# Kernel optimization log

Measured on AMD Instinct MI355X. Metric: run time of the kernel, lower is better.

Reference implementation:

```python
import jax, jax.numpy as jnp
import numpy as np

LN_EPS = 1e-5


def _layernorm(h, g, b):
    mu = jnp.mean(h, axis=-1, keepdims=True)
    var = jnp.var(h, axis=-1, keepdims=True)
    return (h - mu) / jnp.sqrt(var + LN_EPS) * g + b


def setup_inputs() -> dict:
    key = jax.random.key(0)
    ks = jax.random.split(key, 16)
    B, N, C, T = 32, 1024, 64, 24
    K, Fc, Ft = 3, 64, 64

    def xav(k, shape):
        lim = (6.0 / (shape[-2] + shape[-1])) ** 0.5
        return jax.random.uniform(k, shape, jnp.float32, -lim, lim)

    return {
        "x": jax.random.normal(ks[0], (B, N, C, T), jnp.float32),
        "cheb": jax.random.normal(ks[1], (K, N, N), jnp.float32) / np.float32(N) ** 0.5,
        "U1": jax.random.uniform(ks[2], (N,), jnp.float32),
        "U2": xav(ks[3], (C, N)),
        "U3": jax.random.uniform(ks[4], (C,), jnp.float32),
        "b_e": xav(ks[5], (1, T, T)),
        "V_e": xav(ks[6], (T, T)),
        "W1": jax.random.uniform(ks[7], (T,), jnp.float32),
        "W2": xav(ks[8], (C, T)),
        "W3": jax.random.uniform(ks[9], (C,), jnp.float32),
        "b_s": xav(ks[10], (1, N, N)),
        "V_s": xav(ks[11], (N, N)),
        "Theta": xav(ks[12], (K, C, Fc)),
        "tc_w": jax.random.normal(ks[13], (Ft, Fc, 1, 3), jnp.float32) * 0.05,
        "tc_b": jnp.zeros((Ft,), jnp.float32),
        "rc_w": jax.random.normal(ks[14], (Ft, C, 1, 1), jnp.float32) * 0.05,
        "rc_b": jnp.zeros((Ft,), jnp.float32),
        "ln_g": jnp.ones((Ft,), jnp.float32),
        "ln_b": jnp.zeros((Ft,), jnp.float32),
    }


def reference(x, cheb, U1, U2, U3, b_e, V_e, W1, W2, W3, b_s, V_s,
              Theta, tc_w, tc_b, rc_w, rc_b, ln_g, ln_b):
    B, N, C, T = x.shape
    K = Theta.shape[0]

    # ---- temporal attention: E (B,T,T), softmax over axis 1 ----
    lhs_t = jnp.einsum('bnct,n->btc', x, U1) @ U2            # (B,T,N)
    rhs_t = jnp.einsum('c,bnct->bnt', U3, x)                 # (B,N,T)
    prod_t = jnp.einsum('btn,bnu->btu', lhs_t, rhs_t)        # (B,T,T)
    E = jnp.einsum('bik,jk->bij', jax.nn.sigmoid(prod_t + b_e), V_e)
    E = jax.nn.softmax(E, axis=1)

    # ---- apply temporal attention ----
    x_TAt = jnp.einsum('bft,btu->bfu', x.reshape(B, N * C, T), E)
    x_TAt = x_TAt.reshape(B, N, C, T)

    # ---- spatial attention: S (B,N,N), softmax over axis 1 ----
    lhs_s = jnp.einsum('bnct,t->bnc', x_TAt, W1) @ W2        # (B,N,T)
    rhs_s = jnp.einsum('c,bnct->btn', W3, x_TAt)             # (B,T,N)
    prod_s = jnp.einsum('bnt,btm->bnm', lhs_s, rhs_s)        # (B,N,N)
    S = jnp.einsum('bik,jk->bij', jax.nn.sigmoid(prod_s + b_s), V_s)
    S = jax.nn.softmax(S, axis=1)

    # ---- K-order Chebyshev conv with spatial attention ----
    out = jnp.zeros((B, N, Theta.shape[2], T), x.dtype)
    for k in range(K):
        Tk_at = cheb[k] * S                                   # (B,N,N)
        # rhs[b,i,c,t] = sum_m Tk_at[b,m,i] * x[b,m,c,t]
        rhs = jnp.einsum('bmi,bmct->bict', Tk_at, x)
        out = out + jnp.einsum('bict,cf->bift', rhs, Theta[k])
    spatial_gcn = jax.nn.relu(out)                            # (B,N,Fc,T)

    # ---- time conv (1x3, pad (0,1)) on (B,Fc,N,T) ----
    tci = jnp.transpose(spatial_gcn, (0, 2, 1, 3))            # (B,Fc,N,T)
    tco = jax.lax.conv_general_dilated(
        tci, tc_w, window_strides=(1, 1), padding=((0, 0), (1, 1)),
        dimension_numbers=('NCHW', 'OIHW', 'NCHW'))
    tco = tco + tc_b[None, :, None, None]
    tco = jnp.transpose(tco, (0, 2, 1, 3))                    # (B,N,Ft,T)

    # ---- residual 1x1 conv on raw x ----
    rci = jnp.transpose(x, (0, 2, 1, 3))                      # (B,C,N,T)
    rco = jax.lax.conv_general_dilated(
        rci, rc_w, window_strides=(1, 1), padding=((0, 0), (0, 0)),
        dimension_numbers=('NCHW', 'OIHW', 'NCHW'))
    rco = rco + rc_b[None, :, None, None]
    rco = jnp.transpose(rco, (0, 2, 1, 3))                    # (B,N,Ft,T)

    out = jax.nn.relu(rco + tco)                              # (B,N,Ft,T)
    out = _layernorm(jnp.transpose(out, (0, 1, 3, 2)), ln_g, ln_b)
    return jnp.transpose(out, (0, 1, 3, 2))                   # (B,N,Ft,T)
```

## Files before the change

### kernel.cpp

```cpp
#include <hip/hip_runtime.h>

typedef __attribute__((ext_vector_type(8))) short short8;
typedef __attribute__((ext_vector_type(4))) float f32x4;

constexpr int B_ = 32;
constexpr int N_ = 1024;
constexpr int C_ = 64;
constexpr int T_ = 24;
constexpr int F_ = 64;
constexpr int CT_ = C_ * T_;
constexpr int KS_ = 3072;

__device__ __forceinline__ float sigmoidf_(float x) {
    return 1.0f / (1.0f + __expf(-x));
}
__device__ __forceinline__ unsigned short f2b(float f) {
    union { float f; unsigned u; } v; v.f = f;
    unsigned r = v.u + 0x7FFFu + ((v.u >> 16) & 1u);
    return (unsigned short)(r >> 16);
}
__device__ __forceinline__ float b2f(unsigned short h) {
    union { unsigned u; float f; } v; v.u = ((unsigned)h) << 16; return v.f;
}
__device__ __forceinline__ void gload_lds16(const unsigned short* g, unsigned short* l) {
    __builtin_amdgcn_global_load_lds(
        (const __attribute__((address_space(1))) unsigned int*)g,
        (__attribute__((address_space(3))) unsigned int*)l, 16, 0, 0);
}

__global__ __launch_bounds__(256) void k_rhs_t(const float* __restrict__ x,
        const float* __restrict__ U3, float* __restrict__ rhs_t) {
    int b = blockIdx.y, n0 = blockIdx.x * 8;
    int tid = threadIdx.x;
    __shared__ float xr[8 * CT_];
    __shared__ float u3s[C_];
    if (tid < C_) u3s[tid] = U3[tid];
    const float4* x4 = (const float4*)(x + ((size_t)(b * N_ + n0)) * CT_);
#pragma unroll
    for (int e = 0; e < 12; ++e) {
        int i4 = e * 256 + tid;
        float4 v = x4[i4];
        int i = i4 * 4;
        xr[i] = v.x; xr[i + 1] = v.y; xr[i + 2] = v.z; xr[i + 3] = v.w;
    }
    __syncthreads();
    if (tid < 192) {
        int n = tid / 24, t = tid % 24;
        const float* xn = xr + n * CT_ + t;
        float acc = 0.f;
#pragma unroll
        for (int c = 0; c < C_; ++c) acc += u3s[c] * xn[c * 24];
        rhs_t[((size_t)(b * N_ + n0 + n)) * T_ + t] = acc;
    }
}

__global__ void k_lhs_partial(const float* __restrict__ x, const float* __restrict__ U1,
                              float* __restrict__ partial) {
    int b = blockIdx.y, chunk = blockIdx.x;
    int tid = threadIdx.x;
    float acc[6] = {0, 0, 0, 0, 0, 0};
    int n0 = chunk * 64;
    for (int nn = 0; nn < 64; ++nn) {
        int n = n0 + nn;
        float u = U1[n];
        const float* xp = x + ((size_t)(b * N_ + n)) * CT_;
#pragma unroll
        for (int e = 0; e < 6; ++e) acc[e] += u * xp[tid + e * 256];
    }
    float* pp = partial + ((size_t)(b * 16 + chunk)) * CT_;
#pragma unroll
    for (int e = 0; e < 6; ++e) pp[tid + e * 256] = acc[e];
}

__global__ void k_lhs_reduce(const float* __restrict__ partial, float* __restrict__ lhs_t0) {
    int idx = blockIdx.x * 256 + threadIdx.x;
    if (idx >= B_ * CT_) return;
    int b = idx / CT_, flat = idx % CT_;
    float acc = 0.f;
#pragma unroll
    for (int ch = 0; ch < 16; ++ch) acc += partial[((size_t)(b * 16 + ch)) * CT_ + flat];
    lhs_t0[idx] = acc;
}

__global__ void k_lhs_t(const float* __restrict__ lhs_t0, const float* __restrict__ U2,
                        float* __restrict__ lhs_t) {
    int idx = blockIdx.x * 256 + threadIdx.x;
    if (idx >= B_ * T_ * N_) return;
    int n2 = idx % N_;
    int t = (idx / N_) % T_;
    int b = idx / (T_ * N_);
    const float* l0 = lhs_t0 + (size_t)b * CT_;
    float acc = 0.f;
#pragma unroll
    for (int c = 0; c < C_; ++c) acc += l0[c * T_ + t] * U2[c * N_ + n2];
    lhs_t[idx] = acc;
}

__global__ void k_temporal_E(const float* __restrict__ lhs_t, const float* __restrict__ rhs_t,
                             const float* __restrict__ b_e, const float* __restrict__ V_e,
                             float* __restrict__ E) {
    int b = blockIdx.x;
    int tid = threadIdx.x;
    int i = tid / T_, u = tid % T_;
    __shared__ float sig[T_][T_];
    __shared__ float e0s[T_][T_];
    __shared__ float mcol[T_], scol[T_];
    const float* lt = lhs_t + (size_t)b * T_ * N_ + (size_t)i * N_;
    const float* rt = rhs_t + (size_t)b * N_ * T_ + u;
    float acc = 0.f;
    for (int n = 0; n < N_; ++n) acc += lt[n] * rt[(size_t)n * T_];
    sig[i][u] = sigmoidf_(acc + b_e[i * T_ + u]);
    __syncthreads();
    int j = u;
    float e0 = 0.f;
#pragma unroll
    for (int kk = 0; kk < T_; ++kk) e0 += sig[i][kk] * V_e[j * T_ + kk];
    e0s[i][j] = e0;
    __syncthreads();
    if (tid < T_) {
        float mx = -1e30f;
        for (int ii = 0; ii < T_; ++ii) mx = fmaxf(mx, e0s[ii][tid]);
        float s = 0.f;
        for (int ii = 0; ii < T_; ++ii) s += __expf(e0s[ii][tid] - mx);
        mcol[tid] = mx; scol[tid] = s;
    }
    __syncthreads();
    E[(size_t)b * T_ * T_ + i * T_ + j] = __expf(e0s[i][j] - mcol[j]) / scol[j];
}

__global__ __launch_bounds__(256) void k_tspatial(const float* __restrict__ x,
        const float* __restrict__ E, const float* __restrict__ W1g,
        const float* __restrict__ W2, const float* __restrict__ W3g,
        float* __restrict__ lhs_s, float* __restrict__ rhs_s,
        unsigned short* __restrict__ xTt) {
    int b = blockIdx.y;
    int n0 = blockIdx.x * 4;
    int tid = threadIdx.x;
    __shared__ float Es[T_ * T_];
    __shared__ float W1s[T_];
    __shared__ float W2s[C_ * T_];
    __shared__ float xr[4][64][25];
    __shared__ float l0s[4][64];
    for (int e = tid; e < T_ * T_; e += 256) Es[e] = E[(size_t)b * T_ * T_ + e];
    for (int e = tid; e < C_ * T_; e += 256) W2s[e] = W2[e];
    if (tid < T_) W1s[tid] = W1g[tid];
    size_t base = ((size_t)b * N_ + n0) * CT_;
    const float4* x4 = (const float4*)(x + base);
#pragma unroll
    for (int i = 0; i < 6; ++i) {
        int e4 = i * 256 + tid;
        float4 v = x4[e4];
        int e = e4 * 4;
        int nl = e / CT_; int rem = e - nl * CT_; int c = rem / 24; int tl = rem - c * 24;
        xr[nl][c][tl] = v.x; xr[nl][c][tl + 1] = v.y;
        xr[nl][c][tl + 2] = v.z; xr[nl][c][tl + 3] = v.w;
    }
    __syncthreads();
    int nl = tid >> 6, c = tid & 63;
    float xv[T_];
#pragma unroll
    for (int t = 0; t < T_; ++t) xv[t] = xr[nl][c][t];
#pragma unroll
    for (int i = 0; i < 24; ++i) {
        int idx = i * 256 + tid;
        int cc = idx & 63, nn = (idx >> 6) & 3, t = idx >> 8;
        xTt[((size_t)(b * T_ + t) * N_ + n0 + nn) * 64 + cc] = f2b(xr[nn][cc][t]);
    }
    float w3 = W3g[c];
    float u[T_];
#pragma unroll
    for (int j = 0; j < T_; ++j) {
        float a = 0.f;
#pragma unroll
        for (int t = 0; t < T_; ++t) a += xv[t] * Es[t * T_ + j];
        u[j] = a;
    }
    float l0 = 0.f;
#pragma unroll
    for (int j = 0; j < T_; ++j) l0 += u[j] * W1s[j];
    __syncthreads();
#pragma unroll
    for (int j = 0; j < T_; ++j) xr[nl][c][j] = w3 * u[j];
    l0s[nl][c] = l0;
    __syncthreads();
    if (tid < 4 * T_) {
        int t = tid % T_, g = tid / T_;
        float racc = 0.f, lacc = 0.f;
        for (int cc = 0; cc < 64; ++cc) {
            racc += xr[g][cc][t];
            lacc += l0s[g][cc] * W2s[cc * T_ + t];
        }
        rhs_s[((size_t)b * T_ + t) * N_ + n0 + g] = racc;
        lhs_s[((size_t)(b * N_ + n0 + g)) * T_ + t] = lacc;
    }
}

__global__ void k_cvt_vs(const float* __restrict__ v, unsigned short* __restrict__ o) {
    int i = blockIdx.x * 256 + threadIdx.x;
    o[i] = f2b(v[i]);
}

__global__ void k_wcat(const float* __restrict__ tc_w, const float* __restrict__ rc_w,
                       unsigned short* __restrict__ Wcat) {
    int i = blockIdx.x * 256 + threadIdx.x;
    if (i >= F_ * 256) return;
    int ft = i >> 8, k = i & 255;
    int sel = k >> 6, c = k & 63;
    float v = (sel < 3) ? tc_w[(ft * C_ + c) * 3 + sel] : rc_w[ft * C_ + c];
    Wcat[i] = f2b(v);
}

__global__ void k_thp(const float* __restrict__ Theta, unsigned short* __restrict__ Thp) {
    int i = blockIdx.x * 256 + threadIdx.x;
    if (i >= 192 * 64) return;
    int kf = i >> 6, c = i & 63;
    int k = kf >> 6, f = kf & 63;
    Thp[i] = f2b(Theta[((size_t)k * 64 + c) * 64 + f]);
}

__global__ __launch_bounds__(256) void k_sig(const float* __restrict__ lhs_s,
        const float* __restrict__ rhs_s, const float* __restrict__ b_s,
        unsigned short* __restrict__ sigA) {
    int b = blockIdx.z, i0 = blockIdx.y * 64, k0 = blockIdx.x * 256;
    int tid = threadIdx.x;
    __shared__ float lh[64 * T_];
    __shared__ float rh[T_][256];
    for (int e = tid; e < 64 * T_; e += 256) lh[e] = lhs_s[((size_t)b * N_ + i0) * T_ + e];
#pragma unroll
    for (int t = 0; t < T_; ++t) rh[t][tid] = rhs_s[((size_t)b * T_ + t) * N_ + k0 + tid];
    __syncthreads();
    int kg = k0 + tid;
    for (int ii = 0; ii < 64; ++ii) {
        float acc = b_s[(size_t)(i0 + ii) * N_ + kg];
#pragma unroll
        for (int t = 0; t < T_; ++t) acc += lh[ii * T_ + t] * rh[t][tid];
        sigA[((size_t)b * N_ + i0 + ii) * N_ + kg] = f2b(sigmoidf_(acc));
    }
}

__global__ __launch_bounds__(256) void k_yTmm(const unsigned short* __restrict__ xTt,
        const unsigned short* __restrict__ Thp, unsigned short* __restrict__ yT) {
    int bt = blockIdx.y;
    int b = bt / T_, t = bt - b * T_;
    int m0 = blockIdx.x * 128;
    int tid = threadIdx.x;
    int lane = tid & 63, wv = tid >> 6;
    __shared__ __align__(16) char smem[50688];
    unsigned short* Asb = (unsigned short*)smem;
    unsigned short* Bsb = (unsigned short*)(smem + 24576);
    unsigned short* Cl  = (unsigned short*)(smem + 24576);
#pragma unroll
    for (int e = 0; e < 6; ++e) {
        int chunk = e * 256 + tid;
        int row = chunk >> 3, slot = chunk & 7;
        int gslot = slot ^ (row & 7);
        gload_lds16(Thp + row * 64 + gslot * 8, &Asb[chunk * 8]);
    }
    const unsigned short* Bg = xTt + ((size_t)bt * N_ + m0) * 64;
#pragma unroll
    for (int e = 0; e < 4; ++e) {
        int chunk = e * 256 + tid;
        int row = chunk >> 3, slot = chunk & 7;
        int gslot = slot ^ (row & 7);
        gload_lds16(Bg + (size_t)row * 64 + gslot * 8, &Bsb[chunk * 8]);
    }
    __syncthreads();

    short8 bf[2][2];
#pragma unroll
    for (int ni = 0; ni < 2; ++ni)
#pragma unroll
        for (int kk = 0; kk < 2; ++kk) {
            int r = wv * 32 + ni * 16 + (lane & 15);
            int slot = (kk * 4 + (lane >> 4)) ^ (r & 7);
            bf[ni][kk] = *(const short8*)&Bsb[r * 64 + slot * 8];
        }
    f32x4 acc[12][2];
#pragma unroll
    for (int mi = 0; mi < 12; ++mi)
#pragma unroll
        for (int ni = 0; ni < 2; ++ni) acc[mi][ni] = (f32x4){0.f, 0.f, 0.f, 0.f};
#pragma unroll
    for (int mi = 0; mi < 12; ++mi) {
        short8 af[2];
#pragma unroll
        for (int kk = 0; kk < 2; ++kk) {
            int r = mi * 16 + (lane & 15);
            int slot = (kk * 4 + (lane >> 4)) ^ (r & 7);
            af[kk] = *(const short8*)&Asb[r * 64 + slot * 8];
        }
#pragma unroll
        for (int kk = 0; kk < 2; ++kk)
#pragma unroll
            for (int ni = 0; ni < 2; ++ni)
                acc[mi][ni] = __builtin_amdgcn_mfma_f32_16x16x32_bf16(
                    af[kk], bf[ni][kk], acc[mi][ni], 0, 0, 0);
    }
#pragma unroll
    for (int h = 0; h < 2; ++h) {
        __syncthreads();
#pragma unroll
        for (int mi2 = 0; mi2 < 6; ++mi2) {
            int mi = h * 6 + mi2;
#pragma unroll
            for (int r = 0; r < 4; ++r) {
                int row = mi2 * 16 + (lane >> 4) * 4 + r;
#pragma unroll
                for (int ni = 0; ni < 2; ++ni)
                    Cl[row * 136 + wv * 32 + ni * 16 + (lane & 15)] = f2b(acc[mi][ni][r]);
            }
        }
        __syncthreads();
#pragma unroll
        for (int e = 0; e < 6; ++e) {
            int idx = e * 256 + tid;
            int row = idx >> 4, seg = idx & 15;
            int kf = h * 96 + row;
            int k = kf >> 6, f = kf & 63;
            uint4 v = *(const uint4*)&Cl[row * 136 + seg * 8];
            *(uint4*)&yT[((size_t)b * CT_ + f * T_ + t) * KS_ + k * N_ + m0 + seg * 8] = v;
        }
    }
}

__global__ void k_smstats(const float* __restrict__ S, float2* __restrict__ mst) {
    int b = blockIdx.y;
    int jj = threadIdx.x % 64;
    int ig = threadIdx.x / 64;
    int j = blockIdx.x * 64 + jj;
    __shared__ float rm[4][64], rs[4][64];
    float m = -1e30f, s = 0.f;
    for (int i = ig; i < N_; i += 4) {
        float v = S[((size_t)b * N_ + i) * N_ + j];
        float mn = fmaxf(m, v);
        s = s * __expf(m - mn) + __expf(v - mn);
        m = mn;
    }
    rm[ig][jj] = m; rs[ig][jj] = s;
    __syncthreads();
    if (ig == 0) {
        float M = rm[0][jj], SS = rs[0][jj];
#pragma unroll
        for (int g = 1; g < 4; ++g) {
            float mg = rm[g][jj];
            float mn = fmaxf(M, mg);
            SS = SS * __expf(M - mn) + rs[g][jj] * __expf(mg - mn);
            M = mn;
        }
        mst[(size_t)b * N_ + j] = make_float2(M, 1.f / SS);
    }
}

__global__ __launch_bounds__(256) void k_chebSt(const float* __restrict__ cheb,
        const float* __restrict__ S, const float2* __restrict__ mst,
        unsigned short* __restrict__ cs) {
    int b = blockIdx.z, i0 = blockIdx.y * 64, m0 = blockIdx.x * 64;
    int tid = threadIdx.x;
    __shared__ float st[64][65];
    __shared__ float cb[64][65];
    __shared__ float2 sst[64];
    if (tid < 64) sst[tid] = mst[(size_t)b * N_ + i0 + tid];
#pragma unroll
    for (int e = 0; e < 4; ++e) {
        int idx4 = e * 256 + tid;
        int mm = idx4 >> 4, ii0 = (idx4 & 15) * 4;
        float4 v = *(const float4*)&S[((size_t)b * N_ + m0 + mm) * N_ + i0 + ii0];
        st[mm][ii0] = v.x; st[mm][ii0 + 1] = v.y; st[mm][ii0 + 2] = v.z; st[mm][ii0 + 3] = v.w;
    }
    for (int k = 0; k < 3; ++k) {
        __syncthreads();
#pragma unroll
        for (int e = 0; e < 4; ++e) {
            int idx4 = e * 256 + tid;
            int mm = idx4 >> 4, ii0 = (idx4 & 15) * 4;
            float4 v = *(const float4*)&cheb[((size_t)k * N_ + m0 + mm) * N_ + i0 + ii0];
            cb[mm][ii0] = v.x; cb[mm][ii0 + 1] = v.y; cb[mm][ii0 + 2] = v.z; cb[mm][ii0 + 3] = v.w;
        }
        __syncthreads();
#pragma unroll
        for (int e = 0; e < 16; ++e) {
            int idx = e * 256 + tid; int mm = idx & 63, ii = idx >> 6;
            float sm = __expf(st[mm][ii] - sst[ii].x) * sst[ii].y;
            cs[((size_t)b * N_ + i0 + ii) * KS_ + k * N_ + m0 + mm] =
                f2b(sm * cb[mm][ii]);
        }
    }
}

__global__ __launch_bounds__(512, 2) void k_gemm256(
        const unsigned short* __restrict__ A, long lda, long sA,
        const unsigned short* __restrict__ Bt, long ldb, long sB,
        float* __restrict__ Cc, long ldc, long sC, int K, int nbx, int nby) {
    __shared__ __align__(16) unsigned short As[2][256 * 64];
    __shared__ __align__(16) unsigned short Bs[2][256 * 64];
    int tid = threadIdx.x;
    int lane = tid & 63, w = tid >> 6;
    int wy = w >> 2, wx = w & 3;

    int nwg = gridDim.x;
    int cpx = nwg >> 3;
    int logical = (blockIdx.x & 7) * cpx + (blockIdx.x >> 3);
    int tpb = nbx * nby;
    int b = logical / tpb;
    int tile = logical % tpb;
    int i0 = (tile / nbx) * 256;
    int j0 = (tile % nbx) * 256;

    const unsigned short* Ab = A + (size_t)b * sA + (size_t)i0 * lda;
    const unsigned short* Bb = Bt + (size_t)b * sB + (size_t)j0 * ldb;

    auto STAGE = [&](int kt, int d) {
        int kof = kt << 6;
#pragma unroll
        for (int e = 0; e < 4; ++e) {
            int chunk = e * 512 + tid;
            int row = chunk >> 3, slot = chunk & 7;
            int gslot = slot ^ (row & 7);
            gload_lds16(Ab + (size_t)row * lda + kof + gslot * 8, &As[d][chunk * 8]);
        }
#pragma unroll
        for (int e = 0; e < 4; ++e) {
            int chunk = e * 512 + tid;
            int row = chunk >> 3, slot = chunk & 7;
            int gslot = slot ^ (row & 7);
            gload_lds16(Bb + (size_t)row * ldb + kof + gslot * 8, &Bs[d][chunk * 8]);
        }
    };
    auto READF = [&](short8* af, short8* bfv,
                     const unsigned short* Asb, const unsigned short* Bsb, int kkb) {
#pragma unroll
        for (int mi = 0; mi < 8; ++mi) {
            int r = wy * 128 + mi * 16 + (lane & 15);
            int slot = (kkb + (lane >> 4)) ^ (r & 7);
            af[mi] = *(const short8*)&Asb[r * 64 + slot * 8];
        }
#pragma unroll
        for (int ni = 0; ni < 4; ++ni) {
            int r = wx * 64 + ni * 16 + (lane & 15);
            int slot = (kkb + (lane >> 4)) ^ (r & 7);
            bfv[ni] = *(const short8*)&Bsb[r * 64 + slot * 8];
        }
    };

    f32x4 acc[8][4];
#pragma unroll
    for (int mi = 0; mi < 8; ++mi)
#pragma unroll
        for (int ni = 0; ni < 4; ++ni) acc[mi][ni] = (f32x4){0.f, 0.f, 0.f, 0.f};

    int nt = K >> 6;
    STAGE(0, 0);
    STAGE(1, 1);
    asm volatile("s_waitcnt vmcnt(8)" ::: "memory");
    __builtin_amdgcn_s_barrier();
    __builtin_amdgcn_sched_barrier(0);

    short8 a0[8], b0[4], a1[8], b1[4];
    READF(a0, b0, As[0], Bs[0], 0);

    for (int kt = 0; kt < nt; ++kt) {
        int cur = kt & 1;
        READF(a1, b1, As[cur], Bs[cur], 4);
        __builtin_amdgcn_s_setprio(1);
#pragma unroll
        for (int mi = 0; mi < 8; ++mi)
#pragma unroll
            for (int ni = 0; ni < 4; ++ni)
                acc[mi][ni] = __builtin_amdgcn_mfma_f32_16x16x32_bf16(
                    a0[mi], b0[ni], acc[mi][ni], 0, 0, 0);
        __builtin_amdgcn_s_setprio(0);
        asm volatile("s_waitcnt lgkmcnt(0)" ::: "memory");
        __builtin_amdgcn_sched_barrier(0);
        __builtin_amdgcn_s_barrier();
        __builtin_amdgcn_sched_barrier(0);
        if (kt + 2 < nt) STAGE(kt + 2, cur);
        __builtin_amdgcn_sched_barrier(0);
        __builtin_amdgcn_s_setprio(1);
#pragma unroll
        for (int mi = 0; mi < 8; ++mi)
#pragma unroll
            for (int ni = 0; ni < 4; ++ni)
                acc[mi][ni] = __builtin_amdgcn_mfma_f32_16x16x32_bf16(
                    a1[mi], b1[ni], acc[mi][ni], 0, 0, 0);
        __builtin_amdgcn_s_setprio(0);
        if (kt + 2 < nt) {
            asm volatile("s_waitcnt vmcnt(8)" ::: "memory");
        } else {
            asm volatile("s_waitcnt vmcnt(0)" ::: "memory");
        }
        __builtin_amdgcn_s_barrier();
        __builtin_amdgcn_sched_barrier(0);
        if (kt + 1 < nt)
            READF(a0, b0, As[cur ^ 1], Bs[cur ^ 1], 0);
    }

    float* Cb = Cc + (size_t)b * sC;
#pragma unroll
    for (int mi = 0; mi < 8; ++mi) {
#pragma unroll
        for (int r = 0; r < 4; ++r) {
            int i = i0 + wy * 128 + mi * 16 + (lane >> 4) * 4 + r;
            float* cp = Cb + (size_t)i * ldc + j0 + wx * 64 + (lane & 15);
#pragma unroll
            for (int ni = 0; ni < 4; ++ni) cp[ni * 16] = acc[mi][ni][r];
        }
    }
}

__global__ __launch_bounds__(256) void k_final(const float* __restrict__ x,
        const float* __restrict__ sgin, const unsigned short* __restrict__ Wcat,
        const float* __restrict__ tc_b, const float* __restrict__ rc_b,
        const float* __restrict__ ln_g, const float* __restrict__ ln_b,
        float* __restrict__ out) {
    int b = blockIdx.y;
    int n0 = blockIdx.x * 4;
    int tid = threadIdx.x;
    int lane = tid & 63, wv = tid >> 6;

    __shared__ __align__(16) char smem[25600];
    unsigned short* sgb = (unsigned short*)smem;
    unsigned short* xb  = (unsigned short*)(smem + 13312);
    float* Cl = (float*)smem;
    __shared__ float tbs[64], gs[64], bbs[64];
    __shared__ float mus[96], rss[96];

    if (tid < 64) {
        tbs[tid] = tc_b[tid] + rc_b[tid];
        gs[tid] = ln_g[tid];
        bbs[tid] = ln_b[tid];
    }
    for (int e = tid; e < 512; e += 256) {
        int nl = e >> 7, r = (e >> 6) & 1, c = e & 63;
        int tt = r ? 25 : 0;
        sgb[(nl * 26 + tt) * 64 + (((c >> 3) ^ (tt & 7)) << 3) + (c & 7)] = 0;
    }
    size_t base = ((size_t)b * N_ + n0) * CT_;
    const float4* sg4 = (const float4*)(sgin + base);
    const float4* xg4 = (const float4*)(x + base);
#pragma unroll
    for (int i = 0; i < 6; ++i) {
        int e4 = i * 256 + tid;
        float4 sv4 = sg4[e4];
        float4 xv4 = xg4[e4];
        int e = e4 * 4;
        int nl = e / CT_;
        int rem = e - nl * CT_;
        int c = rem / 24;
        int tl = rem - c * 24;
        float sv[4] = {sv4.x, sv4.y, sv4.z, sv4.w};
        float xv[4] = {xv4.x, xv4.y, xv4.z, xv4.w};
#pragma unroll
        for (int j = 0; j < 4; ++j) {
            int tt = tl + j + 1;
            sgb[(nl * 26 + tt) * 64 + (((c >> 3) ^ (tt & 7)) << 3) + (c & 7)] =
                f2b(fmaxf(sv[j], 0.f));
            int tj = tl + j;
            xb[(nl * 24 + tj) * 64 + (((c >> 3) ^ (tj & 7)) << 3) + (c & 7)] = f2b(xv[j]);
        }
    }

    int ft = wv * 16 + (lane & 15);
    int g4 = lane >> 4;
    short8 bfr[8];
#pragma unroll
    for (int ks = 0; ks < 8; ++ks)
        bfr[ks] = *(const short8*)&Wcat[ft * 256 + ks * 32 + g4 * 8];

    int rnl[6], rt[6];
#pragma unroll
    for (int mi = 0; mi < 6; ++mi) {
        int row = mi * 16 + (lane & 15);
        rnl[mi] = row / 24;
        rt[mi] = row - rnl[mi] * 24;
    }

    __syncthreads();

    f32x4 acc[6];
#pragma unroll
    for (int mi = 0; mi < 6; ++mi) acc[mi] = (f32x4){0.f, 0.f, 0.f, 0.f};
#pragma unroll
    for (int mi = 0; mi < 6; ++mi) {
        int nl = rnl[mi], t = rt[mi];
#pragma unroll
        for (int ks = 0; ks < 8; ++ks) {
            const int sel = ks >> 1;
            int slot = (ks & 1) * 4 + g4;
            short8 af;
            if (sel < 3) {
                int tt = t + sel;
                af = *(const short8*)&sgb[(nl * 26 + tt) * 64 + ((slot ^ (tt & 7)) << 3)];
            } else {
                af = *(const short8*)&xb[(nl * 24 + t) * 64 + ((slot ^ (t & 7)) << 3)];
            }
            acc[mi] = __builtin_amdgcn_mfma_f32_16x16x32_bf16(af, bfr[ks], acc[mi], 0, 0, 0);
        }
    }

    __syncthreads();
#pragma unroll
    for (int mi = 0; mi < 6; ++mi)
#pragma unroll
        for (int r = 0; r < 4; ++r)
            Cl[(mi * 16 + (lane >> 4) * 4 + r) * 66 + wv * 16 + (lane & 15)] = acc[mi][r];
    __syncthreads();

    if (tid < 96) {
        float s = 0.f, s2 = 0.f;
#pragma unroll
        for (int f = 0; f < 64; ++f) {
            float v = fmaxf(Cl[tid * 66 + f] + tbs[f], 0.f);
            s += v; s2 += v * v;
        }
        float mu = s * (1.f / 64.f);
        float var = s2 * (1.f / 64.f) - mu * mu;
        mus[tid] = mu;
        rss[tid] = rsqrtf(var + 1e-5f);
    }
    __syncthreads();

    float4* o4 = (float4*)(out + base);
#pragma unroll
    for (int i = 0; i < 6; ++i) {
        int e4 = i * 256 + tid;
        int e = e4 * 4;
        int nl = e / CT_;
        int rem = e - nl * CT_;
        int f = rem / 24;
        int t0v = rem - f * 24;
        float g = gs[f], bb2 = bbs[f], tb2 = tbs[f];
        float vals[4];
#pragma unroll
        for (int j = 0; j < 4; ++j) {
            int row = nl * 24 + t0v + j;
            float v = fmaxf(Cl[row * 66 + f] + tb2, 0.f);
            vals[j] = (v - mus[row]) * rss[row] * g + bb2;
        }
        float4 r;
        r.x = vals[0]; r.y = vals[1]; r.z = vals[2]; r.w = vals[3];
        o4[e4] = r;
    }
}

extern "C" void kernel_launch(void* const* d_in, const int* in_sizes, int n_in,
                              void* d_out, int out_size, void* d_ws, size_t ws_size,
                              hipStream_t stream) {
    const float* x    = (const float*)d_in[0];
    const float* cheb = (const float*)d_in[1];
    const float* U1   = (const float*)d_in[2];
    const float* U2   = (const float*)d_in[3];
    const float* U3   = (const float*)d_in[4];
    const float* b_e  = (const float*)d_in[5];
    const float* V_e  = (const float*)d_in[6];
    const float* W1   = (const float*)d_in[7];
    const float* W2   = (const float*)d_in[8];
    const float* W3   = (const float*)d_in[9];
    const float* b_s  = (const float*)d_in[10];
    const float* V_s  = (const float*)d_in[11];
    const float* Theta= (const float*)d_in[12];
    const float* tc_w = (const float*)d_in[13];
    const float* tc_b = (const float*)d_in[14];
    const float* rc_w = (const float*)d_in[15];
    const float* rc_b = (const float*)d_in[16];
    const float* ln_g = (const float*)d_in[17];
    const float* ln_b = (const float*)d_in[18];
    float* out = (float*)d_out;

    char* base = (char*)d_ws;
    size_t o = 0;
    auto alloc = [&](size_t bytes) { size_t r = o; o += (bytes + 255) & ~(size_t)255; return r; };
    float* lhs_t   = (float*)(base + alloc((size_t)B_ * T_ * N_ * 4));
    float* rhs_t   = (float*)(base + alloc((size_t)B_ * N_ * T_ * 4));
    float* Ebuf    = (float*)(base + alloc((size_t)B_ * T_ * T_ * 4));
    float* partial = (float*)(base + alloc((size_t)B_ * 16 * CT_ * 4));
    float* lhs_t0  = (float*)(base + alloc((size_t)B_ * CT_ * 4));
    float* lhs_s   = (float*)(base + alloc((size_t)B_ * N_ * T_ * 4));
    float* rhs_s   = (float*)(base + alloc((size_t)B_ * T_ * N_ * 4));
    unsigned short* V_sb = (unsigned short*)(base + alloc((size_t)N_ * N_ * 2));
    unsigned short* Wcat = (unsigned short*)(base + alloc((size_t)F_ * 256 * 2));
    unsigned short* Thp  = (unsigned short*)(base + alloc((size_t)192 * 64 * 2));
    float2* mstats = (float2*)(base + alloc((size_t)B_ * N_ * 8));
    size_t regA = alloc((size_t)B_ * N_ * KS_ * 2);
    size_t regB = alloc((size_t)B_ * CT_ * KS_ * 2);
    unsigned short* xTt    = (unsigned short*)(base + regA);
    unsigned short* chebSt = (unsigned short*)(base + regA);
    unsigned short* sigA   = (unsigned short*)(base + regB);
    unsigned short* yT     = (unsigned short*)(base + regB);
    float* Sb  = out;
    float* gcn = out;

    dim3 b256(256);
    k_cvt_vs<<<dim3(N_ * N_ / 256), b256, 0, stream>>>(V_s, V_sb);
    k_wcat<<<dim3((F_ * 256 + 255) / 256), b256, 0, stream>>>(tc_w, rc_w, Wcat);
    k_thp<<<dim3((192 * 64 + 255) / 256), b256, 0, stream>>>(Theta, Thp);
    k_rhs_t<<<dim3(N_ / 8, B_), b256, 0, stream>>>(x, U3, rhs_t);
    k_lhs_partial<<<dim3(16, B_), b256, 0, stream>>>(x, U1, partial);
    k_lhs_reduce<<<dim3((B_ * CT_) / 256), b256, 0, stream>>>(partial, lhs_t0);
    k_lhs_t<<<dim3((B_ * T_ * N_) / 256), b256, 0, stream>>>(lhs_t0, U2, lhs_t);
    k_temporal_E<<<dim3(B_), dim3(576), 0, stream>>>(lhs_t, rhs_t, b_e, V_e, Ebuf);
    k_tspatial<<<dim3(N_ / 4, B_), b256, 0, stream>>>(x, Ebuf, W1, W2, W3,
                                                      lhs_s, rhs_s, xTt);
    k_sig<<<dim3(N_ / 256, N_ / 64, B_), b256, 0, stream>>>(lhs_s, rhs_s, b_s, sigA);
    k_gemm256<<<dim3(B_ * 4 * 4), dim3(512), 0, stream>>>(
        sigA, N_, (long)N_ * N_, V_sb, N_, 0, Sb, N_, (long)N_ * N_, N_, 4, 4);
    k_smstats<<<dim3(N_ / 64, B_), b256, 0, stream>>>(Sb, mstats);
    k_yTmm<<<dim3(N_ / 128, B_ * T_), b256, 0, stream>>>(xTt, Thp, yT);
    k_chebSt<<<dim3(N_ / 64, N_ / 64, B_), b256, 0, stream>>>(cheb, Sb, mstats, chebSt);
    k_gemm256<<<dim3(B_ * 4 * 6), dim3(512), 0, stream>>>(
        chebSt, KS_, (long)N_ * KS_, yT, KS_, (long)CT_ * KS_,
        gcn, CT_, (long)N_ * CT_, KS_, 6, 4);
    k_final<<<dim3(N_ / 4, B_), b256, 0, stream>>>(x, gcn, Wcat, tc_b, rc_b,
                                                   ln_g, ln_b, out);
}
```

Baseline: 1.154 ms.

## Fuse x reductions into one pass and parallelize temporal product over chunks

Merges the U3 and U1 reductions over x into a single kernel that stages x tiles in shared memory, so the large x tensor is read once instead of twice. The prod_t contraction over N is moved out of the 32-block temporal kernel into a chunked kernel with 8 chunks per batch, and the small partials are summed before the sigmoid and softmax. This adds a kernel launch and a larger partial buffer, and gives the fused kernel fewer blocks.

New measurement: 1.067 ms. 7.6% less time.

```diff
diff --git a/kernel.cpp b/kernel.cpp
--- a/kernel.cpp
+++ b/kernel.cpp
@@ -28,48 +28,46 @@
         (__attribute__((address_space(3))) unsigned int*)l, 16, 0, 0);
 }
 
-__global__ __launch_bounds__(256) void k_rhs_t(const float* __restrict__ x,
-        const float* __restrict__ U3, float* __restrict__ rhs_t) {
-    int b = blockIdx.y, n0 = blockIdx.x * 8;
+__global__ __launch_bounds__(256) void k_xreduce(const float* __restrict__ x,
+        const float* __restrict__ U1, const float* __restrict__ U3,
+        float* __restrict__ rhs_t, float* __restrict__ partial) {
+    int b = blockIdx.y, g0 = blockIdx.x * 32;
     int tid = threadIdx.x;
     __shared__ float xr[8 * CT_];
     __shared__ float u3s[C_];
     if (tid < C_) u3s[tid] = U3[tid];
-    const float4* x4 = (const float4*)(x + ((size_t)(b * N_ + n0)) * CT_);
-#pragma unroll
-    for (int e = 0; e < 12; ++e) {
-        int i4 = e * 256 + tid;
-        float4 v = x4[i4];
-        int i = i4 * 4;
-        xr[i] = v.x; xr[i + 1] = v.y; xr[i + 2] = v.z; xr[i + 3] = v.w;
-    }
-    __syncthreads();
-    if (tid < 192) {
-        int n = tid / 24, t = tid % 24;
-        const float* xn = xr + n * CT_ + t;
-        float acc = 0.f;
-#pragma unroll
-        for (int c = 0; c < C_; ++c) acc += u3s[c] * xn[c * 24];
-        rhs_t[((size_t)(b * N_ + n0 + n)) * T_ + t] = acc;
-    }
-}
-
-__global__ void k_lhs_partial(const float* __restrict__ x, const float* __restrict__ U1,
-                              float* __restrict__ partial) {
-    int b = blockIdx.y, chunk = blockIdx.x;
-    int tid = threadIdx.x;
-    float acc[6] = {0, 0, 0, 0, 0, 0};
-    int n0 = chunk * 64;
-    for (int nn = 0; nn < 64; ++nn) {
-        int n = n0 + nn;
-        float u = U1[n];
-        const float* xp = x + ((size_t)(b * N_ + n)) * CT_;
-#pragma unroll
-        for (int e = 0; e < 6; ++e) acc[e] += u * xp[tid + e * 256];
-    }
-    float* pp = partial + ((size_t)(b * 16 + chunk)) * CT_;
-#pragma unroll
-    for (int e = 0; e < 6; ++e) pp[tid + e * 256] = acc[e];
+    float pacc[6] = {0, 0, 0, 0, 0, 0};
+    for (int ph = 0; ph < 4; ++ph) {
+        int n0 = g0 + ph * 8;
+        __syncthreads();
+        const float4* x4 = (const float4*)(x + ((size_t)(b * N_ + n0)) * CT_);
+#pragma unroll
+        for (int e = 0; e < 12; ++e) {
+            int i4 = e * 256 + tid;
+            float4 v = x4[i4];
+            int i = i4 * 4;
+            xr[i] = v.x; xr[i + 1] = v.y; xr[i + 2] = v.z; xr[i + 3] = v.w;
+        }
+        __syncthreads();
+        if (tid < 192) {
+            int n = tid / 24, t = tid % 24;
+            const float* xn = xr + n * CT_ + t;
+            float acc = 0.f;
+#pragma unroll
+            for (int c = 0; c < C_; ++c) acc += u3s[c] * xn[c * 24];
+            rhs_t[((size_t)(b * N_ + n0 + n)) * T_ + t] = acc;
+        }
+#pragma unroll
+        for (int n = 0; n < 8; ++n) {
+            float u = U1[n0 + n];
+            const float* xn = xr + n * CT_;
+#pragma unroll
+            for (int e = 0; e < 6; ++e) pacc[e] += u * xn[tid + e * 256];
+        }
+    }
+    float* pp = partial + ((size_t)(b * 32 + blockIdx.x)) * CT_;
+#pragma unroll
+    for (int e = 0; e < 6; ++e) pp[tid + e * 256] = pacc[e];
 }
 
 __global__ void k_lhs_reduce(const float* __restrict__ partial, float* __restrict__ lhs_t0) {
@@ -78,7 +76,7 @@
     int b = idx / CT_, flat = idx % CT_;
     float acc = 0.f;
 #pragma unroll
-    for (int ch = 0; ch < 16; ++ch) acc += partial[((size_t)(b * 16 + ch)) * CT_ + flat];
+    for (int ch = 0; ch < 32; ++ch) acc += partial[((size_t)(b * 32 + ch)) * CT_ + flat];
     lhs_t0[idx] = acc;
 }
 
@@ -96,7 +94,31 @@
     lhs_t[idx] = acc;
 }
 
-__global__ void k_temporal_E(const float* __restrict__ lhs_t, const float* __restrict__ rhs_t,
+__global__ __launch_bounds__(576) void k_prodt(const float* __restrict__ lhs_t,
+        const float* __restrict__ rhs_t, float* __restrict__ ptp) {
+    int b = blockIdx.y, ch = blockIdx.x;
+    int tid = threadIdx.x;
+    __shared__ float lt[24][128];
+    __shared__ float rt[128][25];
+    int n0 = ch * 128;
+    for (int e = tid; e < 24 * 128; e += 576) {
+        int i = e >> 7, nn = e & 127;
+        lt[i][nn] = lhs_t[((size_t)b * T_ + i) * N_ + n0 + nn];
+    }
+    const float* rg = rhs_t + ((size_t)b * N_ + n0) * T_;
+    for (int e = tid; e < 128 * 24; e += 576) {
+        int nn = e / 24, t = e - nn * 24;
+        rt[nn][t] = rg[e];
+    }
+    __syncthreads();
+    int i = tid / 24, u = tid - (tid / 24) * 24;
+    float acc = 0.f;
+#pragma unroll 8
+    for (int nn = 0; nn < 128; ++nn) acc += lt[i][nn] * rt[nn][u];
+    ptp[(((size_t)b * 8 + ch) * 24 + i) * 24 + u] = acc;
+}
+
+__global__ void k_temporal_E(const float* __restrict__ ptp,
                              const float* __restrict__ b_e, const float* __restrict__ V_e,
                              float* __restrict__ E) {
     int b = blockIdx.x;
@@ -105,10 +127,10 @@
     __shared__ float sig[T_][T_];
     __shared__ float e0s[T_][T_];
     __shared__ float mcol[T_], scol[T_];
-    const float* lt = lhs_t + (size_t)b * T_ * N_ + (size_t)i * N_;
-    const float* rt = rhs_t + (size_t)b * N_ * T_ + u;
     float acc = 0.f;
-    for (int n = 0; n < N_; ++n) acc += lt[n] * rt[(size_t)n * T_];
+#pragma unroll
+    for (int ch = 0; ch < 8; ++ch)
+        acc += ptp[(((size_t)b * 8 + ch) * 24 + i) * 24 + u];
     sig[i][u] = sigmoidf_(acc + b_e[i * T_ + u]);
     __syncthreads();
     int j = u;
@@ -672,7 +694,8 @@
     float* lhs_t   = (float*)(base + alloc((size_t)B_ * T_ * N_ * 4));
     float* rhs_t   = (float*)(base + alloc((size_t)B_ * N_ * T_ * 4));
     float* Ebuf    = (float*)(base + alloc((size_t)B_ * T_ * T_ * 4));
-    float* partial = (float*)(base + alloc((size_t)B_ * 16 * CT_ * 4));
+    float* partial = (float*)(base + alloc((size_t)B_ * 32 * CT_ * 4));
+    float* ptp     = (float*)(base + alloc((size_t)B_ * 8 * T_ * T_ * 4));
     float* lhs_t0  = (float*)(base + alloc((size_t)B_ * CT_ * 4));
     float* lhs_s   = (float*)(base + alloc((size_t)B_ * N_ * T_ * 4));
     float* rhs_s   = (float*)(base + alloc((size_t)B_ * T_ * N_ * 4));
@@ -693,11 +716,11 @@
     k_cvt_vs<<<dim3(N_ * N_ / 256), b256, 0, stream>>>(V_s, V_sb);
     k_wcat<<<dim3((F_ * 256 + 255) / 256), b256, 0, stream>>>(tc_w, rc_w, Wcat);
     k_thp<<<dim3((192 * 64 + 255) / 256), b256, 0, stream>>>(Theta, Thp);
-    k_rhs_t<<<dim3(N_ / 8, B_), b256, 0, stream>>>(x, U3, rhs_t);
-    k_lhs_partial<<<dim3(16, B_), b256, 0, stream>>>(x, U1, partial);
-    k_lhs_reduce<<<dim3((B_ * CT_) / 256), b256, 0, stream>>>(partial, lhs_t0);
+    k_xreduce<<<dim3(N_ / 32, B_), b256, 0, stream>>>(x, U1, U3, rhs_t, partial);
+    k_lhs_reduce<<<dim3((B_ * CT_ + 255) / 256), b256, 0, stream>>>(partial, lhs_t0);
     k_lhs_t<<<dim3((B_ * T_ * N_) / 256), b256, 0, stream>>>(lhs_t0, U2, lhs_t);
-    k_temporal_E<<<dim3(B_), dim3(576), 0, stream>>>(lhs_t, rhs_t, b_e, V_e, Ebuf);
+    k_prodt<<<dim3(8, B_), dim3(576), 0, stream>>>(lhs_t, rhs_t, ptp);
+    k_temporal_E<<<dim3(B_), dim3(576), 0, stream>>>(ptp, b_e, V_e, Ebuf);
     k_tspatial<<<dim3(N_ / 4, B_), b256, 0, stream>>>(x, Ebuf, W1, W2, W3,
                                                       lhs_s, rhs_s, xTt);
     k_sig<<<dim3(N_ / 256, N_ / 64, B_), b256, 0, stream>>>(lhs_s, rhs_s, b_s, sigA);
```
